# Kernel tuning notes

Hardware: AMD Instinct MI355X
Metric: run time of the kernel (lower is better)

Reference implementation:

```python
import jax, jax.numpy as jnp
import numpy as np

K = 7        # kernal_size
STRIDE = 1
PAD = 3      # padding (reflect)
M = K // 2   # center tap index
GAMA = 0.5
EPS = 1e-09


def interp_linear(x, n_out):
    # torch F.interpolate(mode='linear', align_corners=False) on last dim. x: (b, c, n_in)
    n_in = x.shape[-1]
    src = (jnp.arange(n_out, dtype=jnp.float32) + 0.5) * (n_in / n_out) - 0.5
    src = jnp.clip(src, 0.0, n_in - 1.0)
    lo = jnp.floor(src).astype(jnp.int32)
    hi = jnp.minimum(lo + 1, n_in - 1)
    w = (src - lo.astype(jnp.float32)).astype(x.dtype)
    return x[..., lo] * (1.0 - w) + x[..., hi] * w


def unfold1d(x, k, s, p):
    # x: (b, c, n) -> windows (b, L, c, k), matching F.unfold's c-major/k-minor layout
    if p > 0:
        x = jnp.pad(x, ((0, 0), (0, 0), (p, p)), mode='reflect')
    n = x.shape[-1]
    L = (n - k) // s + 1
    idx = jnp.arange(L)[:, None] * s + jnp.arange(k)[None, :]  # (L, k)
    win = x[:, :, idx]                                          # (b, c, L, k)
    return jnp.transpose(win, (0, 2, 1, 3))                     # (b, L, c, k)


def setup_inputs() -> dict:
    key = jax.random.key(0)
    k1, k2, k3, k4, k5 = jax.random.split(key, 5)
    b, dc, nd = 16, 16, 1024
    c_in, c_out, n = 64, 128, 4096
    deep = jax.random.normal(k1, (b, dc, nd), dtype=jnp.float32)
    x = jax.random.normal(k2, (b, c_in, n), dtype=jnp.float32)
    conv_w = jax.random.normal(k3, (c_in, dc), dtype=jnp.float32) * (1.0 / np.sqrt(dc))
    conv_b = jax.random.normal(k4, (c_in,), dtype=jnp.float32) * 0.02
    fc_w = jax.random.normal(k5, (c_out, c_in * K), dtype=jnp.float32) * (1.0 / np.sqrt(c_in * K))
    return {"deep": deep, "x": x, "conv_w": conv_w, "conv_b": conv_b, "fc_w": fc_w}


def reference(deep, x, conv_w, conv_b, fc_w):
    b, c, n = x.shape
    # --- get_deep_loss ---
    xr = interp_linear(deep, n)                                  # (b, dc, n)
    y = jnp.einsum('bdn,cd->bcn', xr, conv_w) + conv_b[None, :, None]
    mean = jnp.mean(y, axis=2, keepdims=True)
    var = jnp.var(y, axis=2, keepdims=True, ddof=1)              # torch var_mean unbiased
    xs = GAMA * (y - mean) / (var + EPS)                         # DeepShuffle1d
    x1 = unfold1d(xs, K, STRIDE, PAD)                            # (b, L, c, k)
    d = jnp.abs(x1 - x1[..., M:M + 1])
    loss = 1.0 - jnp.tanh(d) ** 2                                # (b, L, c, k)
    alpha = 1.0 / jnp.sum(loss, axis=-1, keepdims=True)          # (b, L, c, 1)
    deep_loss = (loss * alpha).reshape(b, -1, c * K)             # (b, L, c*k)
    # --- deep_conv ---
    y1 = unfold1d(x, K, STRIDE, PAD).reshape(b, -1, c * K)       # (b, L, c*k)
    out = jnp.einsum('blf,of->bol', deep_loss * y1, fc_w)        # (b, c_out, L)
    return out
```

## Files before the change

kernel.cpp:

```cpp
#include <hip/hip_runtime.h>
#include <hip/hip_bf16.h>
#include <math.h>

namespace {
typedef __attribute__((ext_vector_type(8)))  short  short8;
typedef __attribute__((ext_vector_type(4)))  float  floatx4;

constexpr int Bc = 16;
constexpr int DC = 16;
constexpr int ND = 1024;
constexpr int C  = 64;
constexpr int N  = 4096;
constexpr int CO = 128;
constexpr int KW = 7;
constexpr int F  = C * KW;
constexpr int LT = 32;
constexpr int PLD = F + 8;
constexpr int GPS = 560;

constexpr size_t WB_OFF = 0;
constexpr size_t GP_OFF = 131072;
constexpr size_t MC_OFF = 417792;
constexpr size_t SC_OFF = 421888;

constexpr float EXP2_SCALE = 2.8853900817779268f;

__device__ inline unsigned short f2bf(float f) {
    __hip_bfloat16 h = __float2bfloat16(f);
    return __builtin_bit_cast(unsigned short, h);
}
__device__ inline float rcpf(float x) { return __builtin_amdgcn_rcpf(x); }

__global__ __launch_bounds__(256)
void k0(const float* __restrict__ deep, const float* __restrict__ fcw,
        unsigned short* __restrict__ wb, float* __restrict__ gp)
{
    __shared__ __align__(16) float Dch[DC][132];
    const int blk = blockIdx.x;
    const int tid = threadIdx.x;

    if (blk < 56) {
        const int i = (blk * 256 + tid) * 4;
        const float4 v = *(const float4*)(fcw + i);
        ushort4 o;
        o.x = f2bf(v.x); o.y = f2bf(v.y); o.z = f2bf(v.z); o.w = f2bf(v.w);
        *(ushort4*)(wb + i) = o;
        return;
    }
    const int i2 = blk - 56;
    const int b  = i2 >> 3;
    const int ch = i2 & 7;
    const int t0 = ch * 128;
    const int d  = tid >> 4;
    const int e  = tid & 15;
#pragma unroll
    for (int p = 0; p < 9; ++p) {
        const int tt = e + 16 * p;
        if (tt < 129)
            Dch[d][tt] = deep[(b * DC + d) * ND + min(t0 + tt, ND - 1)];
    }
    __syncthreads();
    float a0 = 0.f, a1 = 0.f, as = 0.f;
    const int n1 = (ch == 7) ? 127 : 128;
    for (int t = 0; t < 128; ++t) {
        const float vd  = Dch[d][t];
        const float ve  = Dch[e][t];
        const float ve1 = (t < n1) ? Dch[e][t + 1] : 0.f;
        a0 = fmaf(vd, ve, a0);
        a1 = fmaf(vd, ve1, a1);
        as += vd;
    }
    float* gpb = gp + (b * 8 + ch) * GPS;
    gpb[tid] = a0;
    gpb[256 + tid] = a1;
    if (e == 0) {
        gpb[512 + d] = as;
        if (ch == 0) gpb[528 + d] = Dch[d][0];
        if (ch == 7) gpb[544 + d] = Dch[d][127];
    }
}

__global__ __launch_bounds__(256)
void ks(const float* __restrict__ gp, const float* __restrict__ conv_w,
        const float* __restrict__ conv_b, float* __restrict__ mcs,
        float* __restrict__ scs)
{
    __shared__ float G0s[256], G1s[256], ss[16], dd0[16], ddN[16], qp[8][64];
    const int b = blockIdx.x, tid = threadIdx.x;
    {
        float a0 = 0.f, a1 = 0.f;
#pragma unroll
        for (int ch = 0; ch < 8; ++ch) {
            const float* gpb = gp + (b * 8 + ch) * GPS;
            a0 += gpb[tid];
            a1 += gpb[256 + tid];
        }
        G0s[tid] = a0; G1s[tid] = a1;
        if (tid < 16) {
            float s = 0.f;
#pragma unroll
            for (int ch = 0; ch < 8; ++ch) s += gp[(b * 8 + ch) * GPS + 512 + tid];
            ss[tid]  = s;
            dd0[tid] = gp[(b * 8 + 0) * GPS + 528 + tid];
            ddN[tid] = gp[(b * 8 + 7) * GPS + 544 + tid];
        }
    }
    __syncthreads();
    const int c = tid & 63, part = tid >> 6;
    float w[DC];
    {
        const float4* wr = (const float4*)(conv_w + c * DC);
#pragma unroll
        for (int p = 0; p < 4; ++p) {
            const float4 v = wr[p];
            w[4 * p] = v.x; w[4 * p + 1] = v.y; w[4 * p + 2] = v.z; w[4 * p + 3] = v.w;
        }
    }
    float q0 = 0.f, q1 = 0.f;
#pragma unroll
    for (int dd = 0; dd < 4; ++dd) {
        const int d = 4 * part + dd;
        float i0 = 0.f, i1 = 0.f;
#pragma unroll
        for (int e = 0; e < DC; ++e) {
            i0 = fmaf(w[e], G0s[d * 16 + e], i0);
            i1 = fmaf(w[e], G1s[d * 16 + e], i1);
        }
        q0 = fmaf(w[d], i0, q0);
        q1 = fmaf(w[d], i1, q1);
    }
    qp[part][c] = q0;
    qp[4 + part][c] = q1;
    __syncthreads();
    if (tid < 64) {
        const float Q0 = qp[0][c] + qp[1][c] + qp[2][c] + qp[3][c];
        const float Q1 = qp[4][c] + qp[5][c] + qp[6][c] + qp[7][c];
        float wS = 0.f, V0 = 0.f, VN = 0.f;
#pragma unroll
        for (int d = 0; d < DC; ++d) {
            wS = fmaf(w[d], ss[d],  wS);
            V0 = fmaf(w[d], dd0[d], V0);
            VN = fmaf(w[d], ddN[d], VN);
        }
        const float cb   = conv_b[c];
        const float mean = wS * (1.f / 1024.f) + cb;
        const float S2   = 2.625f * Q0 + 1.375f * Q1 + 0.6875f * (V0 * V0 + VN * VN)
                         + 8.f * cb * wS + 4096.f * cb * cb;
        const float var  = (S2 - 4096.f * mean * mean) * (1.f / 4095.f);
        mcs[b * 64 + c] = wS * (1.f / 1024.f);
        scs[b * 64 + c] = (0.5f / (var + 1e-9f)) * EXP2_SCALE;
    }
}

__global__ __launch_bounds__(256, 4)
void k2(const float* __restrict__ deep, const float* __restrict__ conv_w,
        const float* __restrict__ x, const float* __restrict__ mcs,
        const float* __restrict__ scs, const unsigned short* __restrict__ wb,
        float* __restrict__ out)
{
    __shared__ __align__(16) unsigned short phi[LT * PLD];
    __shared__ __align__(16) float Dw[12 * 16];
    const int b   = blockIdx.y;
    const int l0  = blockIdx.x * LT;
    const int t0  = l0 >> 2;
    const int tid = threadIdx.x;
    const int c   = tid & 63;
    const int seg = tid >> 6;

    if (tid < 192) {
        const int ti = tid >> 4, d = tid & 15;
        const int t = min(max(t0 - 2 + ti, 0), ND - 1);
        Dw[ti * 16 + d] = deep[(b * DC + d) * ND + t];
    }
    float w[DC];
    {
        const float4* wr = (const float4*)(conv_w + c * DC);
#pragma unroll
        for (int p = 0; p < 4; ++p) {
            const float4 v = wr[p];
            w[4 * p] = v.x; w[4 * p + 1] = v.y; w[4 * p + 2] = v.z; w[4 * p + 3] = v.w;
        }
    }
    const float mc  = mcs[b * 64 + c];
    const float sc2 = scs[b * 64 + c];
    __syncthreads();

    {
        const int base = l0 + seg * 8;
        float Vr[6];
#pragma unroll
        for (int m = 0; m < 6; ++m) {
            const float* dr = Dw + (2 * seg + m) * 16;
            float a = 0.f;
#pragma unroll
            for (int d = 0; d < DC; ++d) a = fmaf(w[d], dr[d], a);
            Vr[m] = a;
        }
        const float WA[4] = {0.375f, 0.125f, 0.875f, 0.625f};
        float xsv[14], xvf[14];
        const bool edge = (blockIdx.x == 0 && seg == 0) ||
                          (blockIdx.x == (N / LT - 1) && seg == 3);
        const float* xr = x + (size_t)(b * C + c) * N;
        if (!edge) {
            const float4 x0 = *(const float4*)(xr + base - 4);
            const float4 x1 = *(const float4*)(xr + base);
            const float4 x2 = *(const float4*)(xr + base + 4);
            const float4 x3 = *(const float4*)(xr + base + 8);
            const float xf[16] = {x0.x, x0.y, x0.z, x0.w, x1.x, x1.y, x1.z, x1.w,
                                  x2.x, x2.y, x2.z, x2.w, x3.x, x3.y, x3.z, x3.w};
#pragma unroll
            for (int i = 0; i < 14; ++i) {
                const int r  = (i + 1) & 3;
                const int ma = ((i + 5) >> 2) - 1 + (r >> 1);
                const float wa = WA[r];
                xsv[i] = (fmaf(wa, Vr[ma], (1.f - wa) * Vr[ma + 1]) - mc) * sc2;
                xvf[i] = xf[1 + i];
            }
        } else {
            const int tbase = t0 + 2 * seg - 2;
#pragma unroll
            for (int i = 0; i < 14; ++i) {
                const int j  = base - 3 + i;
                const int ja = (j < 0) ? -j : j;
                const int jr = min(ja, 2 * N - 2 - ja);
                const int t  = jr >> 2;
                const int r  = jr & 3;
                const float wa = WA[r];
                int tA = t - 1 + (r >> 1);
                int tB = tA + 1;
                if (tA < 0) { tA = 0; tB = 0; }
                if (tB > ND - 1) tB = ND - 1;
                const int ia = tA - tbase;
                const int ib = tB - tbase;
                xsv[i] = (wa * Vr[ia] + (1.f - wa) * Vr[ib] - mc) * sc2;
                xvf[i] = xr[jr];
            }
        }
        unsigned short* pcol = phi + c * KW;
#pragma unroll
        for (int li = 0; li < 8; ++li) {
            const float cen = xsv[li + 3];
            float u[KW];
            float s = 0.25f;
            u[3] = 0.25f;
#pragma unroll
            for (int k = 0; k < KW; ++k) {
                if (k == 3) continue;
                const float d = fabsf(xsv[li + k] - cen);
                const float e = __builtin_amdgcn_exp2f(-d);
                const float t = 1.f + e;
                const float uk = e * rcpf(t * t);
                u[k] = uk;
                s += uk;
            }
            const float al = rcpf(s);
            unsigned short* pr = pcol + (seg * 8 + li) * PLD;
#pragma unroll
            for (int k = 0; k < KW; ++k) pr[k] = f2bf(u[k] * al * xvf[li + k]);
        }
    }
    __syncthreads();

    const int lane = tid & 63;
    const int quad = lane >> 4;
    const int rr   = lane & 15;
    const int o0   = seg * 32;

    floatx4 acc00 = {0.f, 0.f, 0.f, 0.f}, acc01 = acc00, acc10 = acc00, acc11 = acc00;
    const unsigned short* wrow0 = wb + (o0 + rr) * F + quad * 8;
    const unsigned short* wrow1 = wrow0 + 16 * F;
    const unsigned short* prow0 = phi + rr * PLD + quad * 8;
    const unsigned short* prow1 = prow0 + 16 * PLD;

    for (int s = 0; s < F / 32; ++s) {
        const int f0 = 32 * s;
        const short8 a0 = *(const short8*)(wrow0 + f0);
        const short8 a1 = *(const short8*)(wrow1 + f0);
        const short8 b0 = *(const short8*)(prow0 + f0);
        const short8 b1 = *(const short8*)(prow1 + f0);
        acc00 = __builtin_amdgcn_mfma_f32_16x16x32_bf16(a0, b0, acc00, 0, 0, 0);
        acc01 = __builtin_amdgcn_mfma_f32_16x16x32_bf16(a0, b1, acc01, 0, 0, 0);
        acc10 = __builtin_amdgcn_mfma_f32_16x16x32_bf16(a1, b0, acc10, 0, 0, 0);
        acc11 = __builtin_amdgcn_mfma_f32_16x16x32_bf16(a1, b1, acc11, 0, 0, 0);
    }

    float* ob = out + (size_t)(b * CO) * N + l0;
#pragma unroll
    for (int i = 0; i < 4; ++i) {
        const int om = quad * 4 + i;
        ob[(o0 + om) * N      + rr     ] = acc00[i];
        ob[(o0 + om) * N      + 16 + rr] = acc01[i];
        ob[(o0 + 16 + om) * N + rr     ] = acc10[i];
        ob[(o0 + 16 + om) * N + 16 + rr] = acc11[i];
    }
}
}

extern "C" void kernel_launch(void* const* d_in, const int* in_sizes, int n_in,
                              void* d_out, int out_size, void* d_ws, size_t ws_size,
                              hipStream_t stream)
{
    const float* deep   = (const float*)d_in[0];
    const float* x      = (const float*)d_in[1];
    const float* conv_w = (const float*)d_in[2];
    const float* conv_b = (const float*)d_in[3];
    const float* fc_w   = (const float*)d_in[4];
    float* out = (float*)d_out;

    unsigned short* wbuf = (unsigned short*)((char*)d_ws + WB_OFF);
    float*          gp   = (float*)((char*)d_ws + GP_OFF);
    float*          mcs  = (float*)((char*)d_ws + MC_OFF);
    float*          scs  = (float*)((char*)d_ws + SC_OFF);

    hipLaunchKernelGGL(k0, dim3(56 + 128), dim3(256), 0, stream,
                       deep, fc_w, wbuf, gp);
    hipLaunchKernelGGL(ks, dim3(Bc), dim3(256), 0, stream,
                       gp, conv_w, conv_b, mcs, scs);
    hipLaunchKernelGGL(k2, dim3(N / LT, Bc), dim3(256), 0, stream,
                       deep, conv_w, x, mcs, scs, wbuf, out);
}
```

Baseline: 134.5 us.

## Pre-swizzle bf16 fc weights into MFMA fragment order for coalesced loads

```diff
diff --git a/kernel.cpp b/kernel.cpp
--- a/kernel.cpp
+++ b/kernel.cpp
@@ -17,6 +17,7 @@
 constexpr int LT = 32;
 constexpr int PLD = F + 8;
 constexpr int GPS = 560;
+constexpr int NS = F / 32;
 
 constexpr size_t WB_OFF = 0;
 constexpr size_t GP_OFF = 131072;
@@ -33,21 +34,35 @@
 
 __global__ __launch_bounds__(256)
 void k0(const float* __restrict__ deep, const float* __restrict__ fcw,
-        unsigned short* __restrict__ wb, float* __restrict__ gp)
+        unsigned short* __restrict__ wbs, float* __restrict__ gp)
 {
     __shared__ __align__(16) float Dch[DC][132];
     const int blk = blockIdx.x;
     const int tid = threadIdx.x;
 
-    if (blk < 56) {
-        const int i = (blk * 256 + tid) * 4;
-        const float4 v = *(const float4*)(fcw + i);
-        ushort4 o;
-        o.x = f2bf(v.x); o.y = f2bf(v.y); o.z = f2bf(v.z); o.w = f2bf(v.w);
-        *(ushort4*)(wb + i) = o;
+    if (blk < 28) {
+        const int g    = blk * 256 + tid;
+        const int lane = g & 63;
+        const int q    = lane >> 4;
+        const int rr   = lane & 15;
+        const int rest = g >> 6;
+        const int t    = rest & 1;
+        const int sw   = rest >> 1;
+        const int s    = sw % NS;
+        const int w    = sw / NS;
+        const int o    = w * 32 + t * 16 + rr;
+        const int f    = s * 32 + q * 8;
+        const float4 v0 = *(const float4*)(fcw + o * F + f);
+        const float4 v1 = *(const float4*)(fcw + o * F + f + 4);
+        short8 h;
+        h[0] = (short)f2bf(v0.x); h[1] = (short)f2bf(v0.y);
+        h[2] = (short)f2bf(v0.z); h[3] = (short)f2bf(v0.w);
+        h[4] = (short)f2bf(v1.x); h[5] = (short)f2bf(v1.y);
+        h[6] = (short)f2bf(v1.z); h[7] = (short)f2bf(v1.w);
+        ((short8*)wbs)[g] = h;
         return;
     }
-    const int i2 = blk - 56;
+    const int i2 = blk - 28;
     const int b  = i2 >> 3;
     const int ch = i2 & 7;
     const int t0 = ch * 128;
@@ -152,10 +167,10 @@
     }
 }
 
-__global__ __launch_bounds__(256, 4)
+__global__ __launch_bounds__(256, 3)
 void k2(const float* __restrict__ deep, const float* __restrict__ conv_w,
         const float* __restrict__ x, const float* __restrict__ mcs,
-        const float* __restrict__ scs, const unsigned short* __restrict__ wb,
+        const float* __restrict__ scs, const unsigned short* __restrict__ wbs,
         float* __restrict__ out)
 {
     __shared__ __align__(16) unsigned short phi[LT * PLD];
@@ -267,15 +282,15 @@
     const int o0   = seg * 32;
 
     floatx4 acc00 = {0.f, 0.f, 0.f, 0.f}, acc01 = acc00, acc10 = acc00, acc11 = acc00;
-    const unsigned short* wrow0 = wb + (o0 + rr) * F + quad * 8;
-    const unsigned short* wrow1 = wrow0 + 16 * F;
+    const short8* wp = (const short8*)wbs + (size_t)seg * (NS * 2 * 64) + lane;
     const unsigned short* prow0 = phi + rr * PLD + quad * 8;
     const unsigned short* prow1 = prow0 + 16 * PLD;
 
-    for (int s = 0; s < F / 32; ++s) {
+#pragma unroll
+    for (int s = 0; s < NS; ++s) {
         const int f0 = 32 * s;
-        const short8 a0 = *(const short8*)(wrow0 + f0);
-        const short8 a1 = *(const short8*)(wrow1 + f0);
+        const short8 a0 = wp[s * 128];
+        const short8 a1 = wp[s * 128 + 64];
         const short8 b0 = *(const short8*)(prow0 + f0);
         const short8 b1 = *(const short8*)(prow1 + f0);
         acc00 = __builtin_amdgcn_mfma_f32_16x16x32_bf16(a0, b0, acc00, 0, 0, 0);
@@ -312,7 +327,7 @@
     float*          mcs  = (float*)((char*)d_ws + MC_OFF);
     float*          scs  = (float*)((char*)d_ws + SC_OFF);
 
-    hipLaunchKernelGGL(k0, dim3(56 + 128), dim3(256), 0, stream,
+    hipLaunchKernelGGL(k0, dim3(28 + 128), dim3(256), 0, stream,
                        deep, fc_w, wbuf, gp);
     hipLaunchKernelGGL(ks, dim3(Bc), dim3(256), 0, stream,
                        gp, conv_w, conv_b, mcs, scs);
```

Measured after the change: 119.1 us. 11.4% less time.
